# Performance work log

Measured on AMD Instinct MI355X. Metric: run time of the kernel, lower is better.

## Reference

```python
import jax, jax.numpy as jnp
import numpy as np

N_CHANNELS = 32
DIM_CAPSULE = 16


def setup_inputs() -> dict:
    key = jax.random.key(0)
    k1, k2, k3 = jax.random.split(key, 3)
    B, H, W, Cin = 32, 56, 56, 256
    d, n = DIM_CAPSULE, N_CHANNELS
    inputs = jax.random.normal(k1, (B, H, W, Cin), dtype=jnp.float32)
    # glorot-ish scale for the 3x3 conv kernel
    convW_1 = jax.random.normal(k2, (3, 3, Cin, d * n), dtype=jnp.float32) * 0.02
    bias_1 = jnp.zeros((d * n,), dtype=jnp.float32)
    CapsAct_W = jax.random.normal(k3, (1, 1, d, d * n), dtype=jnp.float32) * 0.1
    CapsAct_B = jnp.zeros((d * n,), dtype=jnp.float32)
    return {"inputs": inputs, "convW_1": convW_1, "bias_1": bias_1,
            "CapsAct_W": CapsAct_W, "CapsAct_B": CapsAct_B}


def reference(inputs, convW_1, bias_1, CapsAct_W, CapsAct_B):
    d, n = DIM_CAPSULE, N_CHANNELS
    # 3x3 stride-2 SAME conv (NHWC / HWIO), bias, relu
    y = jax.lax.conv_general_dilated(
        inputs, convW_1, window_strides=(2, 2), padding="SAME",
        dimension_numbers=("NHWC", "HWIO", "NHWC"))
    y = jax.nn.relu(y + bias_1)                      # [B, Ho, Wo, d*n]
    B, Ho, Wo, _ = y.shape
    # Per-channel 1x1 convs == grouped matmul over capsule channels.
    yg = y.reshape(B, Ho, Wo, n, d)                  # group channels: [B,Ho,Wo,n,d_in]
    Wg = CapsAct_W.reshape(d, n, d)                  # [d_in, n, d_out]
    bg = CapsAct_B.reshape(n, d)                     # [n, d_out]
    # output layout matches tf: [B, Ho, Wo, dim_capsule, n_channels]
    out = jnp.einsum("bhwnd,dne->bhwen", yg, Wg) + bg.T[None, None, None]
    return out
```

## Files before the change

kernel.cpp:

```cpp
#include <hip/hip_runtime.h>
#include <hip/hip_bf16.h>

typedef __attribute__((ext_vector_type(4))) float f32x4;
typedef __attribute__((ext_vector_type(8))) short s16x8;
typedef __attribute__((ext_vector_type(8))) unsigned short u16x8;
typedef __attribute__((ext_vector_type(4))) unsigned short u16x4;

__device__ __forceinline__ unsigned short bfbits(float f) {
  unsigned int u = __builtin_bit_cast(unsigned int, f);
  return (unsigned short)((u + 0x8000u) >> 16);
}

__device__ __forceinline__ void gll16(void* lds, const void* g) {
  __builtin_amdgcn_global_load_lds(
      (const __attribute__((address_space(1))) unsigned int*)g,
      (__attribute__((address_space(3))) unsigned int*)lds, 16, 0, 0);
}

__global__ __launch_bounds__(256)
void prep_all(const float* __restrict__ in, __hip_bfloat16* __restrict__ dst,
              const float* __restrict__ w, __hip_bfloat16* __restrict__ wt) {
  int t = threadIdx.x;
  if (blockIdx.x < 1824) {
    __shared__ __align__(16) unsigned short row[14848];
    int bh = blockIdx.x;
    int h = bh % 57, b = bh / 57;
    __hip_bfloat16* d = (__hip_bfloat16*)dst + (long)bh * 14848;
    if (h < 56) {
      if (t < 64) {
        int par = t >> 5, cq = t & 31;
        u16x4 z = {0, 0, 0, 0};
        *(u16x4*)(row + (par * 32 + cq) * 232 + 224) = z;
        *(u16x4*)(row + (par * 32 + cq) * 232 + 228) = z;
      }
      const float* src = in + (long)(b * 56 + h) * 56 * 256;
#pragma unroll
      for (int j = 0; j < 14; ++j) {
        int idx = j * 256 + t;
        f32x4 v = *(const f32x4*)(src + idx * 4);
        int e0 = idx * 4;
        int ww = e0 >> 8, c = e0 & 255;
        int off = ((ww & 1) * 32 + (c >> 3)) * 232 + (ww >> 1) * 8 + (c & 7);
        u16x4 q = {bfbits(v[0]), bfbits(v[1]), bfbits(v[2]), bfbits(v[3])};
        *(u16x4*)(row + off) = q;
      }
      __syncthreads();
      for (int i = t; i < 1856; i += 256)
        *(u16x8*)(d + i * 8) = *(const u16x8*)(row + i * 8);
    } else {
      u16x8 z = {0, 0, 0, 0, 0, 0, 0, 0};
      for (int i = t; i < 1856; i += 256) *(u16x8*)(d + i * 8) = z;
    }
  } else {
    int u = (blockIdx.x - 1824) * 256 + t;
    int n = u & 511;
    int c8 = (u >> 9) & 31;
    int kpos = u >> 14;
    int tt = kpos * 8 + (c8 >> 2);
    int cq = c8 & 3;
    const float* src = w + ((kpos * 256 + c8 * 8) * 512) + n;
    u16x8 d;
#pragma unroll
    for (int j = 0; j < 8; ++j) d[j] = bfbits(src[j * 512]);
    int nb = n >> 7, nl = n & 127;
    *reinterpret_cast<u16x8*>(wt + ((tt * 4 + nb) * 4096 + cq * 1024 + nl * 8)) = d;
  }
}

__global__ __launch_bounds__(512, 4)
void caps_main_fast(const __hip_bfloat16* __restrict__ inp,
                    const __hip_bfloat16* __restrict__ wt,
                    const float* __restrict__ bias1,
                    const float* __restrict__ capsW,
                    const float* __restrict__ capsB,
                    float* __restrict__ out) {
  __shared__ __align__(16) unsigned char smem[65536];
  __hip_bfloat16* smem_e = (__hip_bfloat16*)smem;

  int bid = (int)blockIdx.x;
  bid = (bid & 7) * 49 + (bid >> 3);
  int mblk = bid >> 2;
  int nb = bid & 3;
  int p0 = mblk * 256;

  int tid = threadIdx.x;
  int lane = tid & 63;
  int wv = tid >> 6;
  int wm = (wv >> 1) * 64;
  int wn = (wv & 1) * 64;
  int col = lane & 15;
  int lq = lane >> 4;

  int bcq = wv >> 1;
  int bnh = wv & 1;
  int ldsB = bcq * 1024 + bnh * 512;

  int baseAf[4];
#pragma unroll
  for (int mf = 0; mf < 4; ++mf) {
    int pA = p0 + wm + 16 * mf + col;
    int bb = pA / 784, rA = pA - bb * 784;
    int hA = rA / 28, wA = rA - hA * 28;
    baseAf[mf] = bb * 846336 + 2 * hA * 14848 + wA * 8 + lq * 232;
  }

  const __hip_bfloat16* wtb = wt + nb * 4096;
  const __hip_bfloat16* bsrc = wtb + bcq * 1024 + bnh * 512 + lane * 8;

  f32x4 acc[4][4] = {};

  gll16(smem_e + ldsB, bsrc);
  __asm__ volatile("s_waitcnt vmcnt(0)" ::: "memory");
  __builtin_amdgcn_s_barrier();
  __asm__ volatile("" ::: "memory");

  int buf = 0;
  for (int t = 0; t < 72; ++t) {
    int kp = t >> 3, tc = t & 7;
    int kh = (kp * 11) >> 5;
    int kw = kp - kh * 3;
    int koff = kh * 14848 + (kw & 1) * 7424 + (kw >> 1) * 8 + tc * 928;
    s16x8 af[4];
#pragma unroll
    for (int mf = 0; mf < 4; ++mf)
      af[mf] = *(const s16x8*)(inp + baseAf[mf] + koff);
    const __hip_bfloat16* sb = smem_e + buf * 4096;
    s16x8 bq[4];
#pragma unroll
    for (int nf = 0; nf < 4; ++nf)
      bq[nf] = *(const s16x8*)(sb + lq * 1024 + (wn + 16 * nf + col) * 8);
    if (t < 71)
      gll16(smem_e + (buf ^ 1) * 4096 + ldsB, bsrc + (t + 1) * 16384);
    __builtin_amdgcn_s_setprio(1);
#pragma unroll
    for (int mf = 0; mf < 4; ++mf)
#pragma unroll
      for (int nf = 0; nf < 4; ++nf)
        acc[mf][nf] = __builtin_amdgcn_mfma_f32_16x16x32_bf16(
            af[mf], bq[nf], acc[mf][nf], 0, 0, 0);
    __builtin_amdgcn_s_setprio(0);
    if (t < 71) {
      __asm__ volatile("s_waitcnt vmcnt(0)" ::: "memory");
      __builtin_amdgcn_s_barrier();
      __asm__ volatile("" ::: "memory");
    }
    buf ^= 1;
  }

  int gb = nb * 8 + (wv & 1) * 4;
  s16x8 wf[4];
  f32x4 cinit[4];
#pragma unroll
  for (int g = 0; g < 4; ++g) {
    int gg = gb + g;
    s16x8 bw = {0, 0, 0, 0, 0, 0, 0, 0};
    if (lq < 2) {
#pragma unroll
      for (int j = 0; j < 8; ++j)
        bw[j] = (short)bfbits(capsW[(8 * lq + j) * 512 + gg * 16 + col]);
    }
    wf[g] = bw;
    float cb = capsB[gg * 16 + col];
    cinit[g] = f32x4{cb, cb, cb, cb};
  }
  float b1v[4];
  int nBase = nb * 128 + wn;
#pragma unroll
  for (int nf = 0; nf < 4; ++nf) b1v[nf] = bias1[nBase + nf * 16 + col];

  __asm__ volatile("s_waitcnt vmcnt(0) lgkmcnt(0)" ::: "memory");
  __builtin_amdgcn_s_barrier();
  __asm__ volatile("" ::: "memory");

  __hip_bfloat16* yw = smem_e + wv * 4096;
#pragma unroll
  for (int nf = 0; nf < 4; ++nf) {
#pragma unroll
    for (int mf = 0; mf < 4; ++mf) {
      f32x4 a = acc[mf][nf];
#pragma unroll
      for (int r = 0; r < 4; ++r) {
        int pl = mf * 16 + lq * 4 + r;
        int nl = nf * 16 + col;
        float v = a[r] + b1v[nf];
        v = v > 0.f ? v : 0.f;
        int off = (pl * 128 + nl * 2) ^ ((pl & 7) << 4);
        *(unsigned short*)((char*)yw + off) = bfbits(v);
      }
    }
  }

#pragma unroll
  for (int mf = 0; mf < 4; ++mf) {
    int prow = 16 * mf + col;
    f32x4 dd[4];
#pragma unroll
    for (int g = 0; g < 4; ++g) {
      s16x8 afv = {0, 0, 0, 0, 0, 0, 0, 0};
      if (lq < 2) {
        int off = (prow * 128 + g * 32 + lq * 16) ^ ((prow & 7) << 4);
        afv = *(const s16x8*)((char*)yw + off);
      }
      dd[g] = __builtin_amdgcn_mfma_f32_16x16x32_bf16(afv, wf[g], cinit[g], 0, 0, 0);
    }
    long pgl = (long)(p0 + wm) + 16 * mf;
#pragma unroll
    for (int r = 0; r < 4; ++r) {
      long pg = pgl + 4 * lq + r;
      f32x4 o = {dd[0][r], dd[1][r], dd[2][r], dd[3][r]};
      *(f32x4*)(out + (pg * 16 + col) * 32 + gb) = o;
    }
  }
}

__global__ __launch_bounds__(256, 3)
void caps_main_v1(const float* __restrict__ in, const __hip_bfloat16* __restrict__ wt,
                  const float* __restrict__ bias1, const float* __restrict__ capsW,
                  const float* __restrict__ capsB, float* __restrict__ out) {
  __shared__ __align__(16) unsigned char smem[32768];
  __hip_bfloat16* sA = (__hip_bfloat16*)smem;
  __hip_bfloat16* sB = (__hip_bfloat16*)(smem + 8192);

  int bid = (int)blockIdx.x;
  bid = (bid & 7) * 98 + (bid >> 3);
  int mblk = bid >> 2;
  int nb = bid & 3;
  int p0 = mblk * 128;

  int tid = threadIdx.x;
  int lane = tid & 63;
  int wv = tid >> 6;
  int wm = (wv >> 1) * 64;
  int wn = (wv & 1) * 64;
  int col = lane & 15;
  int lq = lane >> 4;

  int am = tid & 127;
  int ah = tid >> 7;
  int p = p0 + am;
  int bb = p / 784;
  int rr = p - bb * 784;
  int ho = rr / 28;
  int wo = rr - ho * 28;

  f32x4 acc[4][4] = {};
  const __hip_bfloat16* wtb = wt + nb * 4096;

  for (int kp = 0; kp < 9; ++kp) {
    int kh = kp / 3;
    int kw = kp - kh * 3;
    int h = 2 * ho + kh, ww = 2 * wo + kw;
    bool valid = (h < 56) && (ww < 56);
    const float* arow = in + (((bb * 56 + h) * 56 + ww) * 256) + ah * 16;
#pragma unroll
    for (int tc = 0; tc < 8; ++tc) {
      int t = kp * 8 + tc;
      __syncthreads();
      const __hip_bfloat16* bsrc = wtb + t * 16384 + tid * 8;
      gll16(sB + (wv * 512), bsrc);
      gll16(sB + 2048 + (wv * 512), bsrc + 2048);
      f32x4 v0, v1, v2, v3;
      if (valid) {
        const f32x4* apv = (const f32x4*)(arow + tc * 32);
        v0 = apv[0]; v1 = apv[1]; v2 = apv[2]; v3 = apv[3];
      } else {
        v0 = f32x4{0.f, 0.f, 0.f, 0.f}; v1 = v0; v2 = v0; v3 = v0;
      }
      u16x8 pk0, pk1;
#pragma unroll
      for (int j = 0; j < 4; ++j) {
        pk0[j] = bfbits(v0[j]); pk0[j + 4] = bfbits(v1[j]);
        pk1[j] = bfbits(v2[j]); pk1[j + 4] = bfbits(v3[j]);
      }
      *(u16x8*)(sA + (ah * 2) * 1024 + am * 8) = pk0;
      *(u16x8*)(sA + (ah * 2 + 1) * 1024 + am * 8) = pk1;
      __syncthreads();
      s16x8 af[4], bfr[4];
#pragma unroll
      for (int mf = 0; mf < 4; ++mf)
        af[mf] = *(const s16x8*)(sA + lq * 1024 + (wm + 16 * mf + col) * 8);
#pragma unroll
      for (int nf = 0; nf < 4; ++nf)
        bfr[nf] = *(const s16x8*)(sB + lq * 1024 + (wn + 16 * nf + col) * 8);
#pragma unroll
      for (int mf = 0; mf < 4; ++mf)
#pragma unroll
        for (int nf = 0; nf < 4; ++nf)
          acc[mf][nf] = __builtin_amdgcn_mfma_f32_16x16x32_bf16(
              af[mf], bfr[nf], acc[mf][nf], 0, 0, 0);
    }
  }

  __syncthreads();

  __hip_bfloat16* yw = (__hip_bfloat16*)smem + wv * 4096;
  int nBase = nb * 128 + wn;
#pragma unroll
  for (int nf = 0; nf < 4; ++nf) {
    float b1v = bias1[nBase + nf * 16 + col];
#pragma unroll
    for (int mf = 0; mf < 4; ++mf) {
      f32x4 a = acc[mf][nf];
#pragma unroll
      for (int r = 0; r < 4; ++r) {
        int pl = mf * 16 + lq * 4 + r;
        int nl = nf * 16 + col;
        float v = a[r] + b1v;
        v = v > 0.f ? v : 0.f;
        int off = (pl * 128 + nl * 2) ^ ((pl & 7) << 4);
        *(unsigned short*)((char*)yw + off) = bfbits(v);
      }
    }
  }

  int gb = nb * 8 + (wv & 1) * 4;
  s16x8 wf[4];
  f32x4 cinit[4];
#pragma unroll
  for (int g = 0; g < 4; ++g) {
    int gg = gb + g;
    s16x8 bw = {0, 0, 0, 0, 0, 0, 0, 0};
    if (lq < 2) {
#pragma unroll
      for (int j = 0; j < 8; ++j)
        bw[j] = (short)bfbits(capsW[(8 * lq + j) * 512 + gg * 16 + col]);
    }
    wf[g] = bw;
    float cb = capsB[gg * 16 + col];
    cinit[g] = f32x4{cb, cb, cb, cb};
  }
#pragma unroll
  for (int mf = 0; mf < 4; ++mf) {
    int prow = 16 * mf + col;
    f32x4 dd[4];
#pragma unroll
    for (int g = 0; g < 4; ++g) {
      s16x8 afv = {0, 0, 0, 0, 0, 0, 0, 0};
      if (lq < 2) {
        int off = (prow * 128 + g * 32 + lq * 16) ^ ((prow & 7) << 4);
        afv = *(const s16x8*)((char*)yw + off);
      }
      dd[g] = __builtin_amdgcn_mfma_f32_16x16x32_bf16(afv, wf[g], cinit[g], 0, 0, 0);
    }
    long pgl = (long)(p0 + wm) + 16 * mf;
#pragma unroll
    for (int r = 0; r < 4; ++r) {
      long pg = pgl + 4 * lq + r;
      f32x4 o = {dd[0][r], dd[1][r], dd[2][r], dd[3][r]};
      *(f32x4*)(out + (pg * 16 + col) * 32 + gb) = o;
    }
  }
}

extern "C" void kernel_launch(void* const* d_in, const int* in_sizes, int n_in,
                              void* d_out, int out_size, void* d_ws, size_t ws_size,
                              hipStream_t stream) {
  const float* inputs = (const float*)d_in[0];
  const float* convW  = (const float*)d_in[1];
  const float* bias1  = (const float*)d_in[2];
  const float* capsW  = (const float*)d_in[3];
  const float* capsB  = (const float*)d_in[4];
  float* out = (float*)d_out;

  __hip_bfloat16* wt = (__hip_bfloat16*)d_ws;
  const size_t IN_OFF = 2621440;
  const size_t NEED = IN_OFF + (size_t)27082752 * 2;

  if (ws_size >= NEED) {
    __hip_bfloat16* inp = (__hip_bfloat16*)((char*)d_ws + IN_OFF);
    prep_all<<<2400, 256, 0, stream>>>(inputs, inp, convW, wt);
    caps_main_fast<<<392, 512, 0, stream>>>(inp, wt, bias1, capsW, capsB, out);
  } else {
    prep_all<<<2400, 256, 0, stream>>>(inputs, (__hip_bfloat16*)d_ws, convW, wt);
    caps_main_v1<<<784, 256, 0, stream>>>(inputs, wt, bias1, capsW, capsB, out);
  }
}
```

Before: 108.9 us.

## Stage activation tiles through LDS with triple buffering, load weights directly

```diff
diff --git a/kernel.cpp b/kernel.cpp
--- a/kernel.cpp
+++ b/kernel.cpp
@@ -91,46 +91,54 @@
   int col = lane & 15;
   int lq = lane >> 4;
 
-  int bcq = wv >> 1;
-  int bnh = wv & 1;
-  int ldsB = bcq * 1024 + bnh * 512;
-
-  int baseAf[4];
-#pragma unroll
-  for (int mf = 0; mf < 4; ++mf) {
-    int pA = p0 + wm + 16 * mf + col;
-    int bb = pA / 784, rA = pA - bb * 784;
-    int hA = rA / 28, wA = rA - hA * 28;
-    baseAf[mf] = bb * 846336 + 2 * hA * 14848 + wA * 8 + lq * 232;
-  }
+  int mq = wv >> 1;
+  int cqa = (wv & 1) * 2;
+
+  int p = p0 + mq * 64 + lane;
+  int b = p / 784;
+  int rr = p - b * 784;
+  int ho = rr / 28;
+  int wo = rr - ho * 28;
+  int base0 = b * 846336 + 2 * ho * 14848 + wo * 8;
 
   const __hip_bfloat16* wtb = wt + nb * 4096;
-  const __hip_bfloat16* bsrc = wtb + bcq * 1024 + bnh * 512 + lane * 8;
 
   f32x4 acc[4][4] = {};
 
-  gll16(smem_e + ldsB, bsrc);
-  __asm__ volatile("s_waitcnt vmcnt(0)" ::: "memory");
-  __builtin_amdgcn_s_barrier();
-  __asm__ volatile("" ::: "memory");
-
-  int buf = 0;
-  for (int t = 0; t < 72; ++t) {
+  auto stage = [&](int buf, int t) {
     int kp = t >> 3, tc = t & 7;
     int kh = (kp * 11) >> 5;
     int kw = kp - kh * 3;
-    int koff = kh * 14848 + (kw & 1) * 7424 + (kw >> 1) * 8 + tc * 928;
+    __hip_bfloat16* sa = smem_e + buf * 8192;
+    const __hip_bfloat16* as =
+        inp + base0 + kh * 14848 + (kw & 1) * 7424 + (kw >> 1) * 8 + (tc * 4 + cqa) * 232;
+    gll16(sa + cqa * 2048 + mq * 512, as);
+    gll16(sa + (cqa + 1) * 2048 + mq * 512, as + 232);
+  };
+
+  stage(0, 0);
+  stage(1, 1);
+  __asm__ volatile("s_waitcnt vmcnt(2)" ::: "memory");
+  __builtin_amdgcn_s_barrier();
+  __asm__ volatile("" ::: "memory");
+
+  int rd = 0;
+  for (int t = 0; t < 72; ++t) {
+    const __hip_bfloat16* sa = smem_e + rd * 8192;
     s16x8 af[4];
 #pragma unroll
     for (int mf = 0; mf < 4; ++mf)
-      af[mf] = *(const s16x8*)(inp + baseAf[mf] + koff);
-    const __hip_bfloat16* sb = smem_e + buf * 4096;
+      af[mf] = *(const s16x8*)(sa + lq * 2048 + (wm + 16 * mf + col) * 8);
+    const __hip_bfloat16* bg = wtb + t * 16384 + lq * 1024;
     s16x8 bq[4];
 #pragma unroll
     for (int nf = 0; nf < 4; ++nf)
-      bq[nf] = *(const s16x8*)(sb + lq * 1024 + (wn + 16 * nf + col) * 8);
-    if (t < 71)
-      gll16(smem_e + (buf ^ 1) * 4096 + ldsB, bsrc + (t + 1) * 16384);
+      bq[nf] = *(const s16x8*)(bg + (wn + 16 * nf + col) * 8);
+    __builtin_amdgcn_sched_barrier(0);
+    if (t + 2 < 72) {
+      int st = rd + 2; if (st >= 3) st -= 3;
+      stage(st, t + 2);
+    }
     __builtin_amdgcn_s_setprio(1);
 #pragma unroll
     for (int mf = 0; mf < 4; ++mf)
@@ -140,11 +148,15 @@
             af[mf], bq[nf], acc[mf][nf], 0, 0, 0);
     __builtin_amdgcn_s_setprio(0);
     if (t < 71) {
-      __asm__ volatile("s_waitcnt vmcnt(0)" ::: "memory");
+      if (t < 70) {
+        __asm__ volatile("s_waitcnt vmcnt(2)" ::: "memory");
+      } else {
+        __asm__ volatile("s_waitcnt vmcnt(0)" ::: "memory");
+      }
       __builtin_amdgcn_s_barrier();
       __asm__ volatile("" ::: "memory");
     }
-    buf ^= 1;
+    rd = (rd + 1 == 3) ? 0 : rd + 1;
   }
 
   int gb = nb * 8 + (wv & 1) * 4;
```

Result: slower. 114.8 us (+5.4%).
